# Performance work log

Hardware: AMD Instinct MI355X
Metric: run time of the kernel (lower is better)

Reference implementation:

```python
import jax, jax.numpy as jnp
import numpy as np

GRAY_LEVELS = 32
DISTANCE = 1
LAMBDA = 1.0
ANGLES = [0.0, np.pi / 4, np.pi / 2, 3 * np.pi / 4]
# skimage graycomatrix offsets: row = round(sin(a)*d), col = round(cos(a)*d)
OFFSETS = [(int(round(np.sin(a) * DISTANCE)), int(round(np.cos(a) * DISTANCE))) for a in ANGLES]

# squared gray-level difference matrix, shared by contrast and homogeneity
_lv = np.arange(GRAY_LEVELS, dtype=np.float32)
_D2 = jnp.asarray((_lv[:, None] - _lv[None, :]) ** 2)


def _glcm_props(q, dr, dc):
    # q: [H, W] int32 quantized image; (dr, dc) static pixel offset
    H, W = q.shape
    r0, r1 = max(0, -dr), H - max(0, dr)
    c0, c1 = max(0, -dc), W - max(0, dc)
    a = q[r0:r1, c0:c1]
    b = q[r0 + dr:r1 + dr, c0 + dc:c1 + dc]
    idx = (a * GRAY_LEVELS + b).ravel()
    hist = jnp.zeros(GRAY_LEVELS * GRAY_LEVELS, jnp.float32).at[idx].add(1.0)
    P = hist.reshape(GRAY_LEVELS, GRAY_LEVELS)
    P = P + P.T                       # symmetric=True
    P = P / jnp.maximum(P.sum(), 1.0)  # normed=True
    contrast = jnp.sum(P * _D2)
    energy = jnp.sqrt(jnp.sum(P * P))
    homogeneity = jnp.sum(P / (1.0 + _D2))
    return jnp.stack([contrast, energy, homogeneity])


def texture_features(img):
    # img: [B, 1, H, W] in [0, 1]
    q = jax.lax.stop_gradient((img[:, 0] * (GRAY_LEVELS - 1)).astype(jnp.int32))
    per_angle = []
    for (dr, dc) in OFFSETS:
        per_angle.append(jax.vmap(lambda qi, dr=dr, dc=dc: _glcm_props(qi, dr, dc))(q))
    return jnp.stack(per_angle, axis=1)  # [B, n_angles, 3]


def setup_inputs() -> dict:
    key = jax.random.key(0)
    kx, ky = jax.random.split(key)
    B, C, H, W = 64, 1, 512, 512
    x = jax.random.uniform(kx, (B, C, H, W), dtype=jnp.float32)
    y = jax.random.uniform(ky, (B, C, H, W), dtype=jnp.float32)
    return {"x": x, "y": y}


def reference(x, y):
    fx = texture_features(x)
    fy = texture_features(y)
    return LAMBDA * jnp.mean(jnp.abs(fx - fy))
```

## Files before the change

### kernel.cpp

```cpp
#include <hip/hip_runtime.h>
#include <math.h>

#define G 32
#define IMG_W 512
#define IMG_H 512
#define NPIX (IMG_W * IMG_H)
#define NIMG 128
#define BAND_ROWS 128

__device__ __forceinline__ int quantize(float v) {
    int q = (int)(v * 31.0f);
    return q > 31 ? 31 : q;
}

__global__ __launch_bounds__(1024) void glcm_hist_kernel(
    const float* __restrict__ x, const float* __restrict__ y,
    unsigned int* __restrict__ ghist)
{
    __shared__ unsigned int hist[4 * G * G];

    const int blk = blockIdx.x;
    const int img = blk >> 2;
    const int band = blk & 3;
    const float* base = (img < 64) ? (x + (size_t)img * NPIX)
                                   : (y + (size_t)(img - 64) * NPIX);
    const int t = threadIdx.x;

    #pragma unroll
    for (int k = 0; k < 4; ++k) hist[t + k * 1024] = 0u;
    __syncthreads();

    unsigned int* h0 = hist;
    unsigned int* h1 = hist + 1024;
    unsigned int* h2 = hist + 2048;
    unsigned int* h3 = hist + 3072;

    const int wave = t >> 6, lane = t & 63;
    const int r0 = band * BAND_ROWS + wave * 8;
    const float* rowp = base + (size_t)r0 * IMG_W + lane * 8;

    int qc[8];
    {
        const float4 f0 = *reinterpret_cast<const float4*>(rowp);
        const float4 f1 = *reinterpret_cast<const float4*>(rowp + 4);
        qc[0] = quantize(f0.x); qc[1] = quantize(f0.y);
        qc[2] = quantize(f0.z); qc[3] = quantize(f0.w);
        qc[4] = quantize(f1.x); qc[5] = quantize(f1.y);
        qc[6] = quantize(f1.z); qc[7] = quantize(f1.w);
    }

    for (int r = r0; r < r0 + 8; ++r) {
        const bool havenext = (r + 1 < IMG_H);
        const int nx0 = __shfl_down(qc[0], 1);
        #pragma unroll
        for (int k = 0; k < 7; ++k)
            atomicAdd(&h0[qc[k] * G + qc[k + 1]], 1u);
        if (lane < 63) atomicAdd(&h0[qc[7] * G + nx0], 1u);

        if (havenext) {
            rowp += IMG_W;
            int qn[8];
            const float4 f0 = *reinterpret_cast<const float4*>(rowp);
            const float4 f1 = *reinterpret_cast<const float4*>(rowp + 4);
            qn[0] = quantize(f0.x); qn[1] = quantize(f0.y);
            qn[2] = quantize(f0.z); qn[3] = quantize(f0.w);
            qn[4] = quantize(f1.x); qn[5] = quantize(f1.y);
            qn[6] = quantize(f1.z); qn[7] = quantize(f1.w);

            const int nqn0 = __shfl_down(qn[0], 1);
            const int pqn7 = __shfl_up(qn[7], 1);
            #pragma unroll
            for (int k = 0; k < 8; ++k)
                atomicAdd(&h2[qc[k] * G + qn[k]], 1u);
            #pragma unroll
            for (int k = 0; k < 7; ++k)
                atomicAdd(&h1[qc[k] * G + qn[k + 1]], 1u);
            if (lane < 63) atomicAdd(&h1[qc[7] * G + nqn0], 1u);
            #pragma unroll
            for (int k = 1; k < 8; ++k)
                atomicAdd(&h3[qc[k] * G + qn[k - 1]], 1u);
            if (lane > 0) atomicAdd(&h3[qc[0] * G + pqn7], 1u);

            #pragma unroll
            for (int k = 0; k < 8; ++k) qc[k] = qn[k];
        }
    }
    __syncthreads();

    unsigned int* gh = ghist + (size_t)img * 4096;
    #pragma unroll
    for (int k = 0; k < 4; ++k) {
        const unsigned int v = hist[t + k * 1024];
        if (v) atomicAdd(&gh[t + k * 1024], v);
    }
}

__global__ __launch_bounds__(1024) void glcm_feat_kernel(
    const unsigned int* __restrict__ ghist, float* __restrict__ feats)
{
    __shared__ float red[4][16][3];
    const int img = blockIdx.x;
    const int t = threadIdx.x;
    const unsigned int* gh = ghist + (size_t)img * 4096;

    const int i = t >> 5, j = t & 31;
    const int d2 = (i - j) * (i - j);
    const float inv = 1.0f / (1.0f + (float)d2);
    const int lane = t & 63, wave = t >> 6;
    #pragma unroll
    for (int a = 0; a < 4; ++a) {
        const float h  = (float)gh[a * 1024 + i * G + j];
        const float ht = (float)gh[a * 1024 + j * G + i];
        float cs = h * (float)d2;
        float hs = h * inv;
        float es = (h + ht) * (h + ht);
        #pragma unroll
        for (int off = 32; off; off >>= 1) {
            cs += __shfl_down(cs, off);
            hs += __shfl_down(hs, off);
            es += __shfl_down(es, off);
        }
        if (lane == 0) { red[a][wave][0] = cs; red[a][wave][1] = hs; red[a][wave][2] = es; }
    }
    __syncthreads();
    if (t < 4) {
        float cs = 0.f, hs = 0.f, es = 0.f;
        for (int w = 0; w < 16; ++w) {
            cs += red[t][w][0]; hs += red[t][w][1]; es += red[t][w][2];
        }
        const float Na = (t == 0 || t == 2) ? 261632.0f : 261121.0f;
        float* o = feats + img * 12 + t * 3;
        o[0] = cs / Na;
        o[1] = sqrtf(es) / (2.0f * Na);
        o[2] = hs / Na;
    }
}

__global__ void loss_kernel(const float* __restrict__ feats, float* __restrict__ out)
{
    const int t = threadIdx.x;
    float s = 0.0f;
    for (int k = t; k < 768; k += 256)
        s += fabsf(feats[k] - feats[768 + k]);
    #pragma unroll
    for (int off = 32; off; off >>= 1) s += __shfl_down(s, off);
    __shared__ float red[4];
    if ((t & 63) == 0) red[t >> 6] = s;
    __syncthreads();
    if (t == 0) out[0] = (red[0] + red[1] + red[2] + red[3]) * (1.0f / 768.0f);
}

extern "C" void kernel_launch(void* const* d_in, const int* in_sizes, int n_in,
                              void* d_out, int out_size, void* d_ws, size_t ws_size,
                              hipStream_t stream) {
    const float* x = (const float*)d_in[0];
    const float* y = (const float*)d_in[1];
    unsigned int* ghist = (unsigned int*)d_ws;
    float* feats = (float*)((char*)d_ws + NIMG * 4096 * 4);
    float* out = (float*)d_out;

    hipMemsetAsync(ghist, 0, (size_t)NIMG * 4096 * 4, stream);
    hipLaunchKernelGGL(glcm_hist_kernel, dim3(NIMG * 4), dim3(1024), 0, stream,
                       x, y, ghist);
    hipLaunchKernelGGL(glcm_feat_kernel, dim3(NIMG), dim3(1024), 0, stream,
                       ghist, feats);
    hipLaunchKernelGGL(loss_kernel, dim3(1), dim3(256), 0, stream, feats, out);
}
```

Measured before the change: 53.08 us.

## Replicate shared histograms into eight packed 16-bit sub-histograms per bin

Measured after the change: 53.46 us. No clear change (+0.7%).

```diff
diff --git a/kernel.cpp b/kernel.cpp
--- a/kernel.cpp
+++ b/kernel.cpp
@@ -17,7 +17,7 @@
     const float* __restrict__ x, const float* __restrict__ y,
     unsigned int* __restrict__ ghist)
 {
-    __shared__ unsigned int hist[4 * G * G];
+    __shared__ unsigned int hist[4 * 1024 * 4];
 
     const int blk = blockIdx.x;
     const int img = blk >> 2;
@@ -27,15 +27,17 @@
     const int t = threadIdx.x;
 
     #pragma unroll
-    for (int k = 0; k < 4; ++k) hist[t + k * 1024] = 0u;
+    for (int k = 0; k < 16; ++k) hist[t + k * 1024] = 0u;
     __syncthreads();
 
-    unsigned int* h0 = hist;
-    unsigned int* h1 = hist + 1024;
-    unsigned int* h2 = hist + 2048;
-    unsigned int* h3 = hist + 3072;
+    const int wave = t >> 6, lane = t & 63;
+    const unsigned int whalf = (lane >> 1) & 3;
+    const unsigned int hval = (lane & 1) ? 0x10000u : 1u;
+    unsigned int* h0 = hist + whalf;
+    unsigned int* h1 = hist + 4096 + whalf;
+    unsigned int* h2 = hist + 8192 + whalf;
+    unsigned int* h3 = hist + 12288 + whalf;
 
-    const int wave = t >> 6, lane = t & 63;
     const int r0 = band * BAND_ROWS + wave * 8;
     const float* rowp = base + (size_t)r0 * IMG_W + lane * 8;
 
@@ -54,8 +56,8 @@
         const int nx0 = __shfl_down(qc[0], 1);
         #pragma unroll
         for (int k = 0; k < 7; ++k)
-            atomicAdd(&h0[qc[k] * G + qc[k + 1]], 1u);
-        if (lane < 63) atomicAdd(&h0[qc[7] * G + nx0], 1u);
+            atomicAdd(&h0[(qc[k] * G + qc[k + 1]) << 2], hval);
+        if (lane < 63) atomicAdd(&h0[(qc[7] * G + nx0) << 2], hval);
 
         if (havenext) {
             rowp += IMG_W;
@@ -70,16 +72,16 @@
             const int nqn0 = __shfl_down(qn[0], 1);
             const int pqn7 = __shfl_up(qn[7], 1);
             #pragma unroll
+            for (int k = 0; k < 7; ++k)
+                atomicAdd(&h1[(qc[k] * G + qn[k + 1]) << 2], hval);
+            if (lane < 63) atomicAdd(&h1[(qc[7] * G + nqn0) << 2], hval);
+            #pragma unroll
             for (int k = 0; k < 8; ++k)
-                atomicAdd(&h2[qc[k] * G + qn[k]], 1u);
-            #pragma unroll
-            for (int k = 0; k < 7; ++k)
-                atomicAdd(&h1[qc[k] * G + qn[k + 1]], 1u);
-            if (lane < 63) atomicAdd(&h1[qc[7] * G + nqn0], 1u);
+                atomicAdd(&h2[(qc[k] * G + qn[k]) << 2], hval);
             #pragma unroll
             for (int k = 1; k < 8; ++k)
-                atomicAdd(&h3[qc[k] * G + qn[k - 1]], 1u);
-            if (lane > 0) atomicAdd(&h3[qc[0] * G + pqn7], 1u);
+                atomicAdd(&h3[(qc[k] * G + qn[k - 1]) << 2], hval);
+            if (lane > 0) atomicAdd(&h3[(qc[0] * G + pqn7) << 2], hval);
 
             #pragma unroll
             for (int k = 0; k < 8; ++k) qc[k] = qn[k];
@@ -89,9 +91,13 @@
 
     unsigned int* gh = ghist + (size_t)img * 4096;
     #pragma unroll
-    for (int k = 0; k < 4; ++k) {
-        const unsigned int v = hist[t + k * 1024];
-        if (v) atomicAdd(&gh[t + k * 1024], v);
+    for (int a = 0; a < 4; ++a) {
+        const uint4 w = *reinterpret_cast<const uint4*>(&hist[a * 4096 + t * 4]);
+        const unsigned int s = (w.x & 0xffffu) + (w.x >> 16)
+                             + (w.y & 0xffffu) + (w.y >> 16)
+                             + (w.z & 0xffffu) + (w.z >> 16)
+                             + (w.w & 0xffffu) + (w.w >> 16);
+        if (s) atomicAdd(&gh[a * 1024 + t], s);
     }
 }
 
```
